# Kernel tuning notes

Hardware: AMD Instinct MI355X
Metric: run time of the kernel (lower is better)

Reference implementation:

```python
import jax, jax.numpy as jnp
import numpy as np

N_NODES = 100000
N_EDGES = 1600000
DIM = 64

def setup_inputs() -> dict:
    key = jax.random.key(0)
    k1, k2, k3 = jax.random.split(key, 3)
    x = jax.random.normal(k1, (N_NODES, DIM), dtype=jnp.float32)
    edge_index = jax.random.randint(k2, (2, N_EDGES), 0, N_NODES, dtype=jnp.int64)
    edge_weight = jax.random.uniform(k3, (N_EDGES,), dtype=jnp.float32)
    return {"x": x, "edge_index": edge_index, "edge_weight": edge_weight}

def reference(x, edge_index, edge_weight):
    # out[row] += x[col] * edge_weight  (edge-weighted gather + scatter-add)
    row, col = edge_index[0], edge_index[1]
    messages = x[col] * edge_weight[:, None]            # [E, dim]
    out = jax.ops.segment_sum(messages, row, num_segments=x.shape[0])  # [N, dim]
    return out
```

## Files before the change

kernel.cpp:

```cpp
#include <hip/hip_runtime.h>
#include <hip/hip_fp16.h>
#include <stdint.h>


typedef unsigned long long ull;
typedef int   v4i __attribute__((ext_vector_type(4)));
typedef float v4f __attribute__((ext_vector_type(4)));
typedef float v2f __attribute__((ext_vector_type(2)));
typedef unsigned char  uchar;

#define RB      32
#define CAP     768
#define PCHUNK  4096
#define BCHUNK  4096
#define SLOTS   48
#define BPAD    16
#define OVF_CAP 65536
#define NSBP    32
#define SBROWS  4096
#define NFB     128

__device__ __forceinline__ unsigned short f2bf(float f) {
    union { float f; unsigned int u; } c;
    c.f = f;
    unsigned int lsb = (c.u >> 16) & 1u;
    c.u += 0x7fffu + lsb;
    return (unsigned short)(c.u >> 16);
}
__device__ __forceinline__ float bf2f(unsigned short u) {
    union { unsigned int u; float f; } c;
    c.u = ((unsigned int)u) << 16;
    return c.f;
}
__device__ __forceinline__ float unpack_w(unsigned v) {
    return __half2float(__ushort_as_half((unsigned short)((v & 0x7fffu) << 1)));
}

__global__ __launch_bounds__(512) void prep(
    const int* __restrict__ ei, const float* __restrict__ ew,
    int* __restrict__ bcnt1, ull* __restrict__ seg1, int cap1,
    int* __restrict__ ovf_cnt, int3* __restrict__ ovf, int E, int nbin,
    const float* __restrict__ x, unsigned short* __restrict__ xb, int n4)
{
    __shared__ int hist[NSBP];
    __shared__ int lstart[NSBP];
    __shared__ int gbase[NSBP];
    __shared__ ull sorted[PCHUNK];
    int t = threadIdx.x;

    if ((int)blockIdx.x >= nbin) {
        int i0 = ((int)blockIdx.x - nbin) * 4096 + t;
#pragma unroll
        for (int k = 0; k < 8; ++k) {
            int i = i0 + k * 512;
            if (i < n4) {
                v4f v = ((const v4f*)x)[i];
                ushort4 o;
                o.x = f2bf(v.x); o.y = f2bf(v.y);
                o.z = f2bf(v.z); o.w = f2bf(v.w);
                ((ushort4*)xb)[i] = o;
            }
        }
        return;
    }

    if (t < NSBP) hist[t] = 0;
    __syncthreads();

    int e0   = blockIdx.x * PCHUNK;
    int nval = E - e0; if (nval > PCHUNK) nval = PCHUNK;
    bool al4 = ((E & 3) == 0);

    int   rk[8];
    uchar sb[8];
    ull   cw[8];
    bool  vd[8];
#pragma unroll
    for (int j = 0; j < 2; ++j) {
        int eb = e0 + (j * 512 + t) * 4;
        v4i r4, c4; v4f w4;
        if (al4 && eb + 3 < E) {
            r4 = *(const v4i*)(ei + eb);
            c4 = *(const v4i*)(ei + E + eb);
            w4 = *(const v4f*)(ew + eb);
        } else {
#pragma unroll
            for (int u = 0; u < 4; ++u) {
                int e = eb + u;
                r4[u] = e < E ? ei[e] : 0;
                c4[u] = e < E ? ei[E + e] : 0;
                w4[u] = e < E ? ew[e] : 0.f;
            }
        }
#pragma unroll
        for (int u = 0; u < 4; ++u) {
            int idx = j * 4 + u;
            int e = eb + u;
            vd[idx] = e < E;
            int b = r4[u] >> 12;
            rk[idx] = vd[idx] ? atomicAdd(&hist[b], 1) : 0;
            sb[idx] = (uchar)b;
            unsigned hw = __half_as_ushort(__float2half(w4[u]));
            cw[idx] = ((ull)hw << 48) | ((ull)(unsigned)r4[u] << 24) |
                      (ull)(unsigned)c4[u];
        }
    }
    __syncthreads();

    if (t < 32) {
        int h = hist[t];
        gbase[t] = h ? atomicAdd(&bcnt1[t * BPAD], h) : 0;
        int s = h;
#pragma unroll
        for (int off = 1; off < 32; off <<= 1) {
            int o = __shfl_up(s, off);
            if (t >= off) s += o;
        }
        lstart[t] = s - h;
    }
    __syncthreads();

#pragma unroll
    for (int j = 0; j < 8; ++j) {
        if (!vd[j]) continue;
        sorted[lstart[sb[j]] + rk[j]] = cw[j];
    }
    __syncthreads();

    for (int i = t; i < nval; i += 512) {
        ull e = sorted[i];
        int b = (int)((e >> 24) & 0x1FFFF) >> 12;
        int loc = gbase[b] + (i - lstart[b]);
        if (loc < cap1) {
            seg1[(size_t)b * cap1 + loc] = e;
        } else {
            int o = atomicAdd(ovf_cnt, 1);
            if (o < OVF_CAP)
                ovf[o] = make_int3((int)((e >> 24) & 0x1FFFF),
                                   (int)(e & 0x1FFFF),
                                   __float_as_int(__half2float(
                                       __ushort_as_half((unsigned short)(e >> 48)))));
        }
    }
}

__global__ __launch_bounds__(512) void bin2(
    const ull* __restrict__ seg1, int cap1, const int* __restrict__ bcnt1,
    int* __restrict__ bcnt, ull* __restrict__ seg2,
    int* __restrict__ ovf_cnt, int3* __restrict__ ovf, int chpersb)
{
    __shared__ int hist[NFB];
    __shared__ int lstart[NFB];
    __shared__ int gbase[NFB];
    __shared__ ull sorted[BCHUNK];
    int t  = threadIdx.x;
    int sb = blockIdx.x / chpersb;
    int ch = blockIdx.x % chpersb;

    int cnt1 = bcnt1[sb * BPAD];
    if (cnt1 > cap1) cnt1 = cap1;
    int s0 = ch * BCHUNK;
    int nval = cnt1 - s0;
    if (nval <= 0) return;
    if (nval > BCHUNK) nval = BCHUNK;

    if (t < NFB) hist[t] = 0;
    __syncthreads();

    const ull* base = seg1 + (size_t)sb * cap1 + s0;

    int   rk[8];
    uchar fb[8];
    ull   cw[8];
    bool  vd[8];
#pragma unroll
    for (int j = 0; j < 8; ++j) {
        int i = t + j * 512;
        vd[j] = i < nval;
        ull e = vd[j] ? base[i] : 0;
        int row = (int)((e >> 24) & 0x1FFFF);
        int f = (row >> 5) & (NFB - 1);
        rk[j] = vd[j] ? atomicAdd(&hist[f], 1) : 0;
        fb[j] = (uchar)f;
        cw[j] = e;
    }
    __syncthreads();

    if (t < 64) {
        int h0 = hist[2 * t], h1 = hist[2 * t + 1];
        int fb0 = sb * NFB + 2 * t;
        gbase[2 * t]     = h0 ? atomicAdd(&bcnt[(fb0)     * BPAD], h0) : 0;
        gbase[2 * t + 1] = h1 ? atomicAdd(&bcnt[(fb0 + 1) * BPAD], h1) : 0;
        int ps = h0 + h1;
        int s = ps;
#pragma unroll
        for (int off = 1; off < 64; off <<= 1) {
            int o = __shfl_up(s, off);
            if (t >= off) s += o;
        }
        int excl = s - ps;
        lstart[2 * t]     = excl;
        lstart[2 * t + 1] = excl + h0;
    }
    __syncthreads();

#pragma unroll
    for (int j = 0; j < 8; ++j) {
        if (!vd[j]) continue;
        sorted[lstart[fb[j]] + rk[j]] = cw[j];
    }
    __syncthreads();

    for (int i = t; i < nval; i += 512) {
        ull e = sorted[i];
        int row = (int)((e >> 24) & 0x1FFFF);
        int f = (row >> 5) & (NFB - 1);
        int loc = gbase[f] + (i - lstart[f]);
        int fbg = sb * NFB + f;
        if (loc < CAP) {
            ull hw = (e >> 48) & 0xFFFF;
            seg2[(size_t)fbg * CAP + loc] =
                (hw << 32) | ((ull)(unsigned)(row & (RB - 1)) << 17) |
                (e & 0x1FFFF);
        } else {
            int o = atomicAdd(ovf_cnt, 1);
            if (o < OVF_CAP)
                ovf[o] = make_int3(row, (int)(e & 0x1FFFF),
                                   __float_as_int(__half2float(
                                       __ushort_as_half((unsigned short)(e >> 48)))));
        }
    }
}

template <bool BF>
__global__ __launch_bounds__(256, 8) void bucket_acc(
    const void* __restrict__ xv, const ull* __restrict__ seg2,
    const int* __restrict__ bcnt, float* __restrict__ out,
    int* __restrict__ ovf_cnt, int3* __restrict__ ovf, int N)
{
    __shared__ int      cur[RB];
    __shared__ unsigned tile[RB * SLOTS];
    int t = threadIdx.x;
    int g = blockIdx.x;
    if (t < RB) cur[t] = 0;
    __syncthreads();

    int c = bcnt[g * BPAD];
    if (c > CAP) c = CAP;
    const ull* b8 = seg2 + (size_t)g * CAP;

    for (int i = t; i < c; i += 256) {
        ull e = b8[i];
        int rl = (int)((e >> 17) & (RB - 1));
        unsigned p4 = ((unsigned)(e & 0x1FFFF) << 15) |
                      ((unsigned)(e >> 33) & 0x7FFF);
        int pos = atomicAdd(&cur[rl], 1);
        if (pos < SLOTS) {
            tile[rl * SLOTS + pos] = p4;
        } else {
            int o = atomicAdd(ovf_cnt, 1);
            if (o < OVF_CAP)
                ovf[o] = make_int3(g * RB + rl, (int)(p4 >> 15),
                                   __float_as_int(unpack_w(p4)));
        }
    }
    __syncthreads();

    if (t < RB) {
        int cc = cur[t];
        if (cc > SLOTS) cc = SLOTS;
        if (cc > 0) {
            int ccp = (cc + 15) & ~15;
            if (ccp > SLOTS) ccp = SLOTS;
            unsigned pad = tile[t * SLOTS] & ~0x7fffu;
            for (int i = cc; i < ccp; ++i) tile[t * SLOTS + i] = pad;
            cur[t] = ccp;
        }
    }
    __syncthreads();

    int wid  = t >> 6;
    int lane = t & 63;
    int half = lane >> 5;
    int dp   = lane & 31;
    const ushort2* x2h = (const ushort2*)xv;
    const float2*  x2f = (const float2*)xv;

    for (int k = 0; k < 8; ++k) {
        int r   = wid * 8 + k;
        int row = g * RB + r;
        int cc  = cur[r];
        const unsigned* tb = &tile[r * SLOTS];

        float ax = 0.0f, ay = 0.0f;
        for (int p = 0; p + 16 <= cc; p += 16) {
            unsigned a[8]; float xx[8], xy[8];
#pragma unroll
            for (int i = 0; i < 8; ++i)
                a[i] = tb[p + 2 * i + half];
#pragma unroll
            for (int i = 0; i < 8; ++i) {
                unsigned off = ((a[i] >> 15) << 5) + dp;
                if (BF) { ushort2 v = x2h[off]; xx[i] = bf2f(v.x); xy[i] = bf2f(v.y); }
                else    { float2  v = x2f[off]; xx[i] = v.x;       xy[i] = v.y; }
            }
#pragma unroll
            for (int i = 0; i < 8; ++i) {
                float w = unpack_w(a[i]);
                ax = fmaf(xx[i], w, ax);
                ay = fmaf(xy[i], w, ay);
            }
        }
        ax += __shfl_xor(ax, 32);
        ay += __shfl_xor(ay, 32);
        if (lane < 32 && row < N) {
            v2f o2; o2.x = ax; o2.y = ay;
            __builtin_nontemporal_store(o2,
                ((v2f*)(out + (((size_t)row) << 6))) + dp);
        }
    }
}

template <bool BF>
__global__ __launch_bounds__(256) void ovf_apply(
    const void* __restrict__ xv, const int* __restrict__ ovf_cnt,
    const int3* __restrict__ ovf, float* __restrict__ out)
{
    int n = *ovf_cnt;
    if (n > OVF_CAP) n = OVF_CAP;
    int wid  = (blockIdx.x * 256 + threadIdx.x) >> 6;
    int lane = threadIdx.x & 63;
    int nw   = gridDim.x * 4;
    for (int o = wid; o < n; o += nw) {
        int3 tt = ovf[o];
        float w = __int_as_float(tt.z);
        size_t off = (((size_t)tt.y) << 6) + lane;
        float x = BF ? bf2f(((const unsigned short*)xv)[off])
                     : ((const float*)xv)[off];
        atomicAdd(&out[(((size_t)tt.x) << 6) + lane], x * w);
    }
}

__global__ __launch_bounds__(256) void scatter_edges(
    const float* __restrict__ x, const int* __restrict__ ei,
    const float* __restrict__ ew, float* __restrict__ out, int E)
{
    long long idx = (long long)blockIdx.x * 256 + threadIdx.x;
    int e = (int)(idx >> 4);
    if (e >= E) return;
    int j = (int)(idx & 15);
    int row = ei[e];
    int col = ei[E + e];
    float w = ew[e];
    v4f v = *(const v4f*)(x + (((size_t)col) << 6) + (j << 2));
    float* op = out + (((size_t)row) << 6) + (j << 2);
    atomicAdd(op + 0, v.x * w);
    atomicAdd(op + 1, v.y * w);
    atomicAdd(op + 2, v.z * w);
    atomicAdd(op + 3, v.w * w);
}

extern "C" void kernel_launch(void* const* d_in, const int* in_sizes, int n_in,
                              void* d_out, int out_size, void* d_ws, size_t ws_size,
                              hipStream_t stream) {
    const float* x  = (const float*)d_in[0];
    const int*   ei = (const int*)d_in[1];
    const float* ew = (const float*)d_in[2];
    float*       out = (float*)d_out;

    int E = in_sizes[2];
    int N = out_size / 64;
    int NB  = (N + RB - 1) / RB;
    int NSB = (N + SBROWS - 1) / SBROWS;

    long long mean1 = (long long)E * SBROWS / (N > 0 ? N : 1);
    int cap1 = (int)(mean1 + mean1 / 20 + BCHUNK);
    cap1 = (cap1 + 1023) & ~1023;
    int chpersb = (cap1 + BCHUNK - 1) / BCHUNK;

    size_t bcnt_base = (size_t)NSBP * BPAD;
    size_t ovfc_base = bcnt_base + (size_t)NB * BPAD;
    size_t ovf_base  = (ovfc_base + 1 + 3) & ~(size_t)3;
    size_t xb_base   = (ovf_base + 3 * (size_t)OVF_CAP + 3) & ~(size_t)3;
    size_t seg1_base = (xb_base + (size_t)N * 32 + 1) & ~(size_t)1;
    size_t seg2_base = seg1_base + (size_t)NSB * cap1 * 2;
    size_t need      = (seg2_base + (size_t)NB * CAP * 2) * 4;

    int nbin  = (E + PCHUNK - 1) / PCHUNK;
    int n4    = (N * 64) / 4;
    int nconv = (n4 + 4095) / 4096;

    if (ws_size >= need && N <= (1 << 17)) {
        int* w32 = (int*)d_ws;
        int* bcnt1   = w32;
        int* bcnt    = w32 + bcnt_base;
        int* ovf_cnt = w32 + ovfc_base;
        int3* ovf    = (int3*)(w32 + ovf_base);
        unsigned short* xb = (unsigned short*)(w32 + xb_base);
        ull* seg1 = (ull*)(w32 + seg1_base);
        ull* seg2 = (ull*)(w32 + seg2_base);

        (void)hipMemsetAsync(w32, 0,
            (bcnt_base + (size_t)NB * BPAD + 2) * sizeof(int), stream);

        prep<<<nbin + nconv, 512, 0, stream>>>(
            ei, ew, bcnt1, seg1, cap1, ovf_cnt, ovf, E, nbin, x, xb, n4);
        bin2<<<NSB * chpersb, 512, 0, stream>>>(
            seg1, cap1, bcnt1, bcnt, seg2, ovf_cnt, ovf, chpersb);
        bucket_acc<true><<<NB, 256, 0, stream>>>(
            xb, seg2, bcnt, out, ovf_cnt, ovf, N);
        ovf_apply<true><<<64, 256, 0, stream>>>(xb, ovf_cnt, ovf, out);
    } else {
        (void)hipMemsetAsync(out, 0, (size_t)out_size * sizeof(float), stream);
        long long threads = (long long)E * 16;
        scatter_edges<<<(int)((threads + 255) / 256), 256, 0, stream>>>(
            x, ei, ew, out, E);
    }
}
```

Before: 163.5 us.

## Replace global-atomic superbin scatter with per-chunk sorted runs gathered in bin2

Measured after the change: 159.7 us. 2.3% less time.

```diff
diff --git a/kernel.cpp b/kernel.cpp
--- a/kernel.cpp
+++ b/kernel.cpp
@@ -12,7 +12,8 @@
 #define RB      32
 #define CAP     768
 #define PCHUNK  4096
-#define BCHUNK  4096
+#define G2MAX   32
+#define TOT2    4608
 #define SLOTS   48
 #define BPAD    16
 #define OVF_CAP 65536
@@ -38,13 +39,11 @@
 
 __global__ __launch_bounds__(512) void prep(
     const int* __restrict__ ei, const float* __restrict__ ew,
-    int* __restrict__ bcnt1, ull* __restrict__ seg1, int cap1,
-    int* __restrict__ ovf_cnt, int3* __restrict__ ovf, int E, int nbin,
+    int* __restrict__ tbl, ull* __restrict__ seg1, int E, int nbin,
     const float* __restrict__ x, unsigned short* __restrict__ xb, int n4)
 {
     __shared__ int hist[NSBP];
     __shared__ int lstart[NSBP];
-    __shared__ int gbase[NSBP];
     __shared__ ull sorted[PCHUNK];
     int t = threadIdx.x;
 
@@ -109,14 +108,15 @@
 
     if (t < 32) {
         int h = hist[t];
-        gbase[t] = h ? atomicAdd(&bcnt1[t * BPAD], h) : 0;
         int s = h;
 #pragma unroll
         for (int off = 1; off < 32; off <<= 1) {
             int o = __shfl_up(s, off);
             if (t >= off) s += o;
         }
-        lstart[t] = s - h;
+        int ls = s - h;
+        lstart[t] = ls;
+        tbl[blockIdx.x * NSBP + t] = (ls << 16) | h;
     }
     __syncthreads();
 
@@ -127,13 +127,101 @@
     }
     __syncthreads();
 
-    for (int i = t; i < nval; i += 512) {
-        ull e = sorted[i];
-        int b = (int)((e >> 24) & 0x1FFFF) >> 12;
-        int loc = gbase[b] + (i - lstart[b]);
-        if (loc < cap1) {
-            seg1[(size_t)b * cap1 + loc] = e;
+    ull* dst = seg1 + (size_t)blockIdx.x * PCHUNK;
+    for (int i = t; i < nval; i += 512) dst[i] = sorted[i];
+}
+
+__global__ __launch_bounds__(512) void bin2(
+    const ull* __restrict__ seg1, const int* __restrict__ tbl, int nbin,
+    int* __restrict__ bcnt, ull* __restrict__ seg2,
+    int* __restrict__ ovf_cnt, int3* __restrict__ ovf,
+    int nblkpersb, int g2)
+{
+    __shared__ int nrun[G2MAX], lsrun[G2MAX], runstart[G2MAX + 1];
+    __shared__ int hist[NFB], lstart[NFB], gbase[NFB];
+    __shared__ ull sorted[TOT2];
+    int t  = threadIdx.x;
+    int sbk = blockIdx.x / nblkpersb;
+    int j   = blockIdx.x % nblkpersb;
+    int c0  = j * g2;
+    int nc  = nbin - c0; if (nc > g2) nc = g2;
+    if (nc <= 0) return;
+
+    if (t < NFB) hist[t] = 0;
+    if (t < G2MAX) {
+        int v = (t < nc) ? tbl[(c0 + t) * NSBP + sbk] : 0;
+        nrun[t]  = v & 0xFFFF;
+        lsrun[t] = v >> 16;
+    }
+    __syncthreads();
+
+    if (t < 32) {
+        int n = nrun[t];
+        int s = n;
+#pragma unroll
+        for (int off = 1; off < 32; off <<= 1) {
+            int o = __shfl_up(s, off);
+            if (t >= off) s += o;
+        }
+        runstart[t] = s - n;
+        if (t == 31) runstart[32] = s;
+    }
+    __syncthreads();
+
+    int total = runstart[G2MAX];
+    if (total > TOT2) total = TOT2;
+
+    int   rk_[9];
+    uchar fb_[9];
+    ull   e_[9];
+#pragma unroll
+    for (int jj = 0; jj < 9; ++jj) {
+        int i = t + jj * 512;
+        bool vd = i < total;
+        ull e = 0;
+        if (vd) {
+            int c = 0;
+#pragma unroll
+            for (int s = 16; s; s >>= 1)
+                if (c + s <= 31 && runstart[c + s] <= i) c += s;
+            e = seg1[(size_t)(c0 + c) * PCHUNK + lsrun[c] +
+                     (i - runstart[c])];
+        }
+        int row = (int)((e >> 24) & 0x1FFFF);
+        int f = (row >> 5) & (NFB - 1);
+        rk_[jj] = vd ? atomicAdd(&hist[f], 1) : 0;
+        fb_[jj] = (uchar)f;
+        e_[jj]  = e;
+    }
+    __syncthreads();
+
+    if (t < 64) {
+        int h0 = hist[2 * t], h1 = hist[2 * t + 1];
+        int fb0 = sbk * NFB + 2 * t;
+        gbase[2 * t]     = h0 ? atomicAdd(&bcnt[(fb0)     * BPAD], h0) : 0;
+        gbase[2 * t + 1] = h1 ? atomicAdd(&bcnt[(fb0 + 1) * BPAD], h1) : 0;
+        int ps = h0 + h1;
+        int s = ps;
+#pragma unroll
+        for (int off = 1; off < 64; off <<= 1) {
+            int o = __shfl_up(s, off);
+            if (t >= off) s += o;
+        }
+        int excl = s - ps;
+        lstart[2 * t]     = excl;
+        lstart[2 * t + 1] = excl + h0;
+    }
+    __syncthreads();
+
+#pragma unroll
+    for (int jj = 0; jj < 9; ++jj) {
+        int i = t + jj * 512;
+        if (i >= total) continue;
+        int idx = lstart[fb_[jj]] + rk_[jj];
+        if (idx < TOT2) {
+            sorted[idx] = e_[jj];
         } else {
+            ull e = e_[jj];
             int o = atomicAdd(ovf_cnt, 1);
             if (o < OVF_CAP)
                 ovf[o] = make_int3((int)((e >> 24) & 0x1FFFF),
@@ -142,81 +230,14 @@
                                        __ushort_as_half((unsigned short)(e >> 48)))));
         }
     }
-}
-
-__global__ __launch_bounds__(512) void bin2(
-    const ull* __restrict__ seg1, int cap1, const int* __restrict__ bcnt1,
-    int* __restrict__ bcnt, ull* __restrict__ seg2,
-    int* __restrict__ ovf_cnt, int3* __restrict__ ovf, int chpersb)
-{
-    __shared__ int hist[NFB];
-    __shared__ int lstart[NFB];
-    __shared__ int gbase[NFB];
-    __shared__ ull sorted[BCHUNK];
-    int t  = threadIdx.x;
-    int sb = blockIdx.x / chpersb;
-    int ch = blockIdx.x % chpersb;
-
-    int cnt1 = bcnt1[sb * BPAD];
-    if (cnt1 > cap1) cnt1 = cap1;
-    int s0 = ch * BCHUNK;
-    int nval = cnt1 - s0;
-    if (nval <= 0) return;
-    if (nval > BCHUNK) nval = BCHUNK;
-
-    if (t < NFB) hist[t] = 0;
-    __syncthreads();
-
-    const ull* base = seg1 + (size_t)sb * cap1 + s0;
-
-    int   rk[8];
-    uchar fb[8];
-    ull   cw[8];
-    bool  vd[8];
-#pragma unroll
-    for (int j = 0; j < 8; ++j) {
-        int i = t + j * 512;
-        vd[j] = i < nval;
-        ull e = vd[j] ? base[i] : 0;
-        int row = (int)((e >> 24) & 0x1FFFF);
-        int f = (row >> 5) & (NFB - 1);
-        rk[j] = vd[j] ? atomicAdd(&hist[f], 1) : 0;
-        fb[j] = (uchar)f;
-        cw[j] = e;
-    }
-    __syncthreads();
-
-    if (t < 64) {
-        int h0 = hist[2 * t], h1 = hist[2 * t + 1];
-        int fb0 = sb * NFB + 2 * t;
-        gbase[2 * t]     = h0 ? atomicAdd(&bcnt[(fb0)     * BPAD], h0) : 0;
-        gbase[2 * t + 1] = h1 ? atomicAdd(&bcnt[(fb0 + 1) * BPAD], h1) : 0;
-        int ps = h0 + h1;
-        int s = ps;
-#pragma unroll
-        for (int off = 1; off < 64; off <<= 1) {
-            int o = __shfl_up(s, off);
-            if (t >= off) s += o;
-        }
-        int excl = s - ps;
-        lstart[2 * t]     = excl;
-        lstart[2 * t + 1] = excl + h0;
-    }
-    __syncthreads();
-
-#pragma unroll
-    for (int j = 0; j < 8; ++j) {
-        if (!vd[j]) continue;
-        sorted[lstart[fb[j]] + rk[j]] = cw[j];
-    }
-    __syncthreads();
-
-    for (int i = t; i < nval; i += 512) {
+    __syncthreads();
+
+    for (int i = t; i < total; i += 512) {
         ull e = sorted[i];
         int row = (int)((e >> 24) & 0x1FFFF);
         int f = (row >> 5) & (NFB - 1);
         int loc = gbase[f] + (i - lstart[f]);
-        int fbg = sb * NFB + f;
+        int fbg = sbk * NFB + f;
         if (loc < CAP) {
             ull hw = (e >> 48) & 0xFFFF;
             seg2[(size_t)fbg * CAP + loc] =
@@ -373,40 +394,43 @@
     int NB  = (N + RB - 1) / RB;
     int NSB = (N + SBROWS - 1) / SBROWS;
 
-    long long mean1 = (long long)E * SBROWS / (N > 0 ? N : 1);
-    int cap1 = (int)(mean1 + mean1 / 20 + BCHUNK);
-    cap1 = (cap1 + 1023) & ~1023;
-    int chpersb = (cap1 + BCHUNK - 1) / BCHUNK;
-
-    size_t bcnt_base = (size_t)NSBP * BPAD;
-    size_t ovfc_base = bcnt_base + (size_t)NB * BPAD;
+    int nbin = (E + PCHUNK - 1) / PCHUNK;
+
+    long long g2ll = ((long long)TOT2 * 85 / 100) * N /
+                     ((long long)PCHUNK * SBROWS);
+    int g2 = (int)g2ll;
+    if (g2 < 1) g2 = 1;
+    if (g2 > G2MAX) g2 = G2MAX;
+    int nblkpersb = (nbin + g2 - 1) / g2;
+
+    size_t ovfc_base = (size_t)NB * BPAD;
     size_t ovf_base  = (ovfc_base + 1 + 3) & ~(size_t)3;
-    size_t xb_base   = (ovf_base + 3 * (size_t)OVF_CAP + 3) & ~(size_t)3;
+    size_t tbl_base  = (ovf_base + 3 * (size_t)OVF_CAP + 3) & ~(size_t)3;
+    size_t xb_base   = tbl_base + (size_t)nbin * NSBP;
     size_t seg1_base = (xb_base + (size_t)N * 32 + 1) & ~(size_t)1;
-    size_t seg2_base = seg1_base + (size_t)NSB * cap1 * 2;
+    size_t seg2_base = seg1_base + (size_t)nbin * PCHUNK * 2;
     size_t need      = (seg2_base + (size_t)NB * CAP * 2) * 4;
 
-    int nbin  = (E + PCHUNK - 1) / PCHUNK;
     int n4    = (N * 64) / 4;
     int nconv = (n4 + 4095) / 4096;
 
     if (ws_size >= need && N <= (1 << 17)) {
         int* w32 = (int*)d_ws;
-        int* bcnt1   = w32;
-        int* bcnt    = w32 + bcnt_base;
+        int* bcnt    = w32;
         int* ovf_cnt = w32 + ovfc_base;
         int3* ovf    = (int3*)(w32 + ovf_base);
+        int* tbl     = w32 + tbl_base;
         unsigned short* xb = (unsigned short*)(w32 + xb_base);
         ull* seg1 = (ull*)(w32 + seg1_base);
         ull* seg2 = (ull*)(w32 + seg2_base);
 
         (void)hipMemsetAsync(w32, 0,
-            (bcnt_base + (size_t)NB * BPAD + 2) * sizeof(int), stream);
+            ((size_t)NB * BPAD + 2) * sizeof(int), stream);
 
         prep<<<nbin + nconv, 512, 0, stream>>>(
-            ei, ew, bcnt1, seg1, cap1, ovf_cnt, ovf, E, nbin, x, xb, n4);
-        bin2<<<NSB * chpersb, 512, 0, stream>>>(
-            seg1, cap1, bcnt1, bcnt, seg2, ovf_cnt, ovf, chpersb);
+            ei, ew, tbl, seg1, E, nbin, x, xb, n4);
+        bin2<<<NSB * nblkpersb, 512, 0, stream>>>(
+            seg1, tbl, nbin, bcnt, seg2, ovf_cnt, ovf, nblkpersb, g2);
         bucket_acc<true><<<NB, 256, 0, stream>>>(
             xb, seg2, bcnt, out, ovf_cnt, ovf, N);
         ovf_apply<true><<<64, 256, 0, stream>>>(xb, ovf_cnt, ovf, out);
```
